# Kernel tuning notes

Measured on AMD Instinct MI355X. Metric: run time of the kernel, lower is better.

The kernel has to match this reference:

```python
import jax, jax.numpy as jnp
import numpy as np

N, E, D = 20000, 640000, 128  # nodes, edges, hidden_nf
ED = 3  # edge_feat_nf (1 input col + distance col + geodesic col)
NORM_FACTOR = 100.0
NORM_CONST = 1.0
LN_EPS = 1e-5


def setup_inputs() -> dict:
    key = jax.random.key(0)
    ks = jax.random.split(key, 24)
    w = lambda k, s: (jax.random.normal(k, s, dtype=jnp.float32) * 0.1)
    inp = {
        "h": jax.random.normal(ks[0], (N, D), dtype=jnp.float32),
        "x": jax.random.normal(ks[1], (N, 3), dtype=jnp.float32),
        "edge_index": jax.random.randint(ks[2], (2, E), 0, N),
        "node_mask": jnp.ones((N, 1), jnp.float32),
        "edge_mask": jnp.ones((E, 1), jnp.float32),
        "edge_attr": jax.random.uniform(ks[3], (E, 1), dtype=jnp.float32),
        # GCLayer params
        "W_lin": w(ks[4], (D, D)), "b_lin": jnp.zeros((D,), jnp.float32),
        "We1": w(ks[5], (D + ED, D)), "be1": jnp.zeros((D,), jnp.float32),
        "We2": w(ks[6], (D, D)), "be2": jnp.zeros((D,), jnp.float32),
        "Wn1": w(ks[7], (D, D)), "bn1": jnp.zeros((D,), jnp.float32),
        "Wn2": w(ks[8], (D, D)), "bn2": jnp.zeros((D,), jnp.float32),
        "Wa1": w(ks[9], (2 * D + ED, D)), "ba1": jnp.zeros((D,), jnp.float32),
        "Wa2": w(ks[10], (D, 1)), "ba2": jnp.zeros((1,), jnp.float32),
        "ln_g": jnp.ones((D,), jnp.float32), "ln_b": jnp.zeros((D,), jnp.float32),
        # EquivariantUpdate coord_mlp params (last layer bias-free, gain 0.001)
        "Wc1": w(ks[11], (2 * D + ED, D)), "bc1": jnp.zeros((D,), jnp.float32),
        "Wc2": w(ks[12], (D, D)), "bc2": jnp.zeros((D,), jnp.float32),
        "Wc3": w(ks[13], (D, 1)) * 0.01,
    }
    return inp


def _forward(h, x, edge_index, node_mask, edge_mask, edge_attr,
             W_lin, b_lin, We1, be1, We2, be2, Wn1, bn1, Wn2, bn2,
             Wa1, ba1, Wa2, ba2, ln_g, ln_b, Wc1, bc1, Wc2, bc2, Wc3):
    silu = jax.nn.silu
    row, col = edge_index[0], edge_index[1]
    # coord2diff
    diff = x[row] - x[col]                                     # [E,3]
    radial = jnp.sum(diff * diff, axis=1, keepdims=True)
    dist = jnp.sqrt(radial + 1e-8)                             # [E,1]
    coord_diff = diff / (dist + NORM_CONST)
    e = jnp.concatenate([dist, edge_attr], axis=1)             # [E,2]
    # ---- GCLayer (Euclidean reduction of HGCLayer) ----
    hh = h @ W_lin + b_lin                                     # [N,D]
    hr, hc = hh[row], hh[col]
    geo = jnp.sqrt(jnp.sum((hr - hc) ** 2, axis=1, keepdims=True) + 1e-8)
    e3 = jnp.concatenate([e, geo], axis=1)                     # [E,3]
    att_in = jnp.concatenate([hr, hc, e3], axis=1)             # [E,2D+3]
    att = jax.nn.sigmoid(silu(att_in @ Wa1 + ba1) @ Wa2 + ba2) * edge_mask
    msg_in = jnp.concatenate([hc - hr, e3], axis=1)            # [E,D+3]
    msg = (silu(msg_in @ We1 + be1) @ We2 + be2) * att
    agg = jax.ops.segment_sum(msg, row, num_segments=hh.shape[0])  # [N,D]
    out = silu(agg @ Wn1 + bn1) @ Wn2 + bn2
    hh = hh + out
    mu = jnp.mean(hh, axis=-1, keepdims=True)
    var = jnp.mean((hh - mu) ** 2, axis=-1, keepdims=True)
    hh = (hh - mu) * jax.lax.rsqrt(var + LN_EPS) * ln_g + ln_b
    hh = silu(hh)
    # ---- EquivariantUpdate (tanh=False) ----
    cin = jnp.concatenate([hh[row], hh[col], e3], axis=1)      # [E,2D+3]
    m = silu(cin @ Wc1 + bc1)
    m = silu(m @ Wc2 + bc2)
    m = m @ Wc3                                                # [E,1]
    trans = coord_diff * m * edge_mask
    aggx = jax.ops.segment_sum(trans, row, num_segments=x.shape[0]) / NORM_FACTOR
    x_out = (x + aggx) * node_mask
    return hh, x_out


def reference(h, x, edge_index, node_mask, edge_mask, edge_attr,
              W_lin, b_lin, We1, be1, We2, be2, Wn1, bn1, Wn2, bn2,
              Wa1, ba1, Wa2, ba2, ln_g, ln_b, Wc1, bc1, Wc2, bc2, Wc3):
    return _forward(h, x, edge_index, node_mask, edge_mask, edge_attr,
                    W_lin, b_lin, We1, be1, We2, be2, Wn1, bn1, Wn2, bn2,
                    Wa1, ba1, Wa2, ba2, ln_g, ln_b, Wc1, bc1, Wc2, bc2, Wc3)
```

## Files before the change

kernel.cpp:

```cpp
#include <hip/hip_runtime.h>
#include <hip/hip_bf16.h>


#define D 128
#define RS 136

typedef unsigned short ushort;
typedef __fp16 half8 __attribute__((ext_vector_type(8)));
typedef __fp16 h16x2 __attribute__((ext_vector_type(2)));
typedef _Float16 f16x2 __attribute__((ext_vector_type(2)));
typedef __attribute__((ext_vector_type(4))) float f32x4;

__device__ __forceinline__ float rcpf(float x) { return __builtin_amdgcn_rcpf(x); }
__device__ __forceinline__ float siluf(float x) { return x * rcpf(1.0f + __expf(-x)); }
__device__ __forceinline__ float sigmf(float x) { return rcpf(1.0f + __expf(-x)); }
__device__ __forceinline__ ushort f2hs(float f) {
    _Float16 h = (_Float16)f; ushort u; __builtin_memcpy(&u, &h, 2); return u;
}
__device__ __forceinline__ unsigned pkh(float lo, float hi) {
    auto h = __builtin_amdgcn_cvt_pkrtz(lo, hi);
    unsigned u; __builtin_memcpy(&u, &h, 4); return u;
}
__device__ __forceinline__ unsigned pksub(unsigned a, unsigned b) {
    f16x2 x, y; __builtin_memcpy(&x, &a, 4); __builtin_memcpy(&y, &b, 4);
    f16x2 d = x - y; unsigned r; __builtin_memcpy(&r, &d, 4); return r;
}
__device__ __forceinline__ float2 up2(unsigned u) {
    f16x2 h; __builtin_memcpy(&h, &u, 4);
    return make_float2((float)h.x, (float)h.y);
}
__device__ __forceinline__ float fdot2f(f16x2 a, f16x2 b, float c) {
#if __has_builtin(__builtin_amdgcn_fdot2)
    h16x2 ah, bh;
    __builtin_memcpy(&ah, &a, 4); __builtin_memcpy(&bh, &b, 4);
    return __builtin_amdgcn_fdot2(ah, bh, c, false);
#else
    return c + (float)a.x * (float)b.x + (float)a.y * (float)b.y;
#endif
}
#define MFMA16(a, b, c) __builtin_amdgcn_mfma_f32_16x16x32_f16((a), (b), (c), 0, 0, 0)

#define PWLIN 0
#define PU    5
#define PV    9
#define PM    13
#define PE2   17
#define PN1   21
#define PN2   26
#define PP    30
#define PQ    34
#define PC2   38
#define NPACK 42

__global__ void k_zero(float* __restrict__ p, long n) {
    long i = (long)blockIdx.x * blockDim.x + threadIdx.x;
    long stride = (long)gridDim.x * blockDim.x;
    for (; i < n; i += stride) p[i] = 0.0f;
}

__global__ void k_hist(const int* __restrict__ eidx, int* __restrict__ cnt, int E) {
    int i = blockIdx.x * blockDim.x + threadIdx.x;
    const int stride = gridDim.x * blockDim.x;
    for (; i < E; i += stride) atomicAdd(&cnt[eidx[i]], 1);
}

__global__ __launch_bounds__(1024) void k_scan(const int* __restrict__ cnt,
                                               int* __restrict__ cur, int N) {
    __shared__ int part[1024];
    const int t = threadIdx.x;
    const int chunk = (N + 1023) / 1024;
    int s = 0;
    for (int k = 0; k < chunk; ++k) {
        const int i = t * chunk + k;
        if (i < N) s += cnt[i];
    }
    part[t] = s;
    __syncthreads();
    for (int d = 1; d < 1024; d <<= 1) {
        const int v = (t >= d) ? part[t - d] : 0;
        __syncthreads();
        part[t] += v;
        __syncthreads();
    }
    int base = (t == 0) ? 0 : part[t - 1];
    for (int k = 0; k < chunk; ++k) {
        const int i = t * chunk + k;
        if (i < N) { cur[i] = base; base += cnt[i]; }
    }
}

__global__ void k_scatter_build(
    const int* __restrict__ eidx, const float* __restrict__ x,
    const float* __restrict__ eattr, const float* __restrict__ emask,
    int* __restrict__ cur, float4* __restrict__ rec, int E) {
    int i = blockIdx.x * blockDim.x + threadIdx.x;
    const int stride = gridDim.x * blockDim.x;
    for (; i < E; i += stride) {
        const int r = eidx[i], c = eidx[E + i];
        const int p = atomicAdd(&cur[r], 1);
        const float dx = x[r * 3 + 0] - x[c * 3 + 0];
        const float dy = x[r * 3 + 1] - x[c * 3 + 1];
        const float dz = x[r * 3 + 2] - x[c * 3 + 2];
        const float dist = sqrtf(dx * dx + dy * dy + dz * dz + 1e-8f);
        const float inv = rcpf(dist + 1.0f);
        rec[2 * p + 0] = make_float4(__int_as_float(r), __int_as_float(c), dist, eattr[i]);
        rec[2 * p + 1] = make_float4(emask[i], dx * inv, dy * inv, dz * inv);
    }
}

__global__ __launch_bounds__(256) void k_packall(
    const float* __restrict__ W_lin, const float* __restrict__ b_lin,
    const float* __restrict__ Wa1,
    const float* __restrict__ We1,
    const float* __restrict__ We2,
    const float* __restrict__ Wn1, const float* __restrict__ bn1,
    const float* __restrict__ Wn2,
    const float* __restrict__ Wc1,
    const float* __restrict__ Wc2,
    ushort* __restrict__ pack) {
    const int b = blockIdx.x, t = threadIdx.x;
    const float* W = nullptr; const float* bias = nullptr;
    int kbase = 0, fold = 0, ext = 0, nW = 0;
    if (b < 5)       { W = W_lin; bias = b_lin; if (b == 4) { ext = 1; nW = 0; } else kbase = b * 32; }
    else if (b < 9)  { W = Wa1; kbase = (b - 5) * 32; fold = 1; }
    else if (b < 13) { W = Wa1; kbase = 128 + (b - 9) * 32; }
    else if (b < 17) { W = We1; kbase = (b - 13) * 32; }
    else if (b < 21) { W = We2; kbase = (b - 17) * 32; }
    else if (b < 26) { int k = b - 21; W = Wn1; bias = bn1; if (k == 4) { ext = 1; nW = 0; } else kbase = k * 32; }
    else if (b < 30) { W = Wn2; kbase = (b - 26) * 32; }
    else if (b < 34) { W = Wc1; kbase = (b - 30) * 32; }
    else if (b < 38) { W = Wc1; kbase = 128 + (b - 34) * 32; }
    else             { W = Wc2; kbase = (b - 38) * 32; }
    ushort* dst = pack + (size_t)b * 4096;
#pragma unroll
    for (int i = 0; i < 16; ++i) {
        const int e = t + 256 * i;
        const int j = e & 7, lane = (e >> 3) & 63, nt = e >> 9;
        const int kl = (lane >> 4) * 8 + j;
        const int n = nt * 16 + (lane & 15);
        float v;
        if (!ext) {
            v = W[(kbase + kl) * D + n];
            if (fold) v += W[(kbase + kl + 128) * D + n];
        } else {
            v = (kl < nW) ? W[(kbase + kl) * D + n] : (kl == nW ? bias[n] : 0.0f);
        }
        dst[e] = f2hs(v);
    }
}

__global__ __launch_bounds__(256) void k_node_lin(
    const float* __restrict__ h, const ushort* __restrict__ pack,
    float* __restrict__ hh, ushort* __restrict__ hh1b,
    float* __restrict__ Uf, ushort* __restrict__ Vh, ushort* __restrict__ Mh,
    const float* __restrict__ ba1f, int N) {
    __shared__ ushort hs[64][RS];
    const int t = threadIdx.x, lane = t & 63, wave = t >> 6;
    const int quad = lane >> 4, l16 = lane & 15;
    const int mh = wave >> 1, nh = wave & 1;
    const int base = blockIdx.x * 64;

#pragma unroll
    for (int q = 0; q < 8; ++q) {
        const int f = t + 256 * q;
        const int row = f >> 5, c4 = (f & 31) << 2;
        const int node = base + row;
        float4 v = make_float4(0.f, 0.f, 0.f, 0.f);
        if (node < N) v = *(const float4*)(h + (size_t)node * D + c4);
        *(uint2*)&hs[row][c4] = make_uint2(pkh(v.x, v.y), pkh(v.z, v.w));
    }
    float ba1v[4];
#pragma unroll
    for (int nt = 0; nt < 4; ++nt) ba1v[nt] = ba1f[nh * 64 + nt * 16 + l16];
    __syncthreads();

    half8 aext = (half8)0;
    if (quad == 0) aext[0] = (__fp16)1.0f;

    f32x4 acc[2][4] = {};
    {
        const half8* pB = (const half8*)(pack + (size_t)PWLIN * 4096);
#pragma unroll
        for (int ks = 0; ks < 5; ++ks) {
            half8 bfr[4];
#pragma unroll
            for (int nt = 0; nt < 4; ++nt) bfr[nt] = pB[(ks * 8 + nh * 4 + nt) * 64 + lane];
#pragma unroll
            for (int mt = 0; mt < 2; ++mt) {
                const half8 a = (ks < 4) ? *(const half8*)&hs[mh * 32 + mt * 16 + l16][ks * 32 + quad * 8]
                                         : aext;
#pragma unroll
                for (int nt = 0; nt < 4; ++nt) acc[mt][nt] = MFMA16(a, bfr[nt], acc[mt][nt]);
            }
        }
    }
    __syncthreads();
#pragma unroll
    for (int mt = 0; mt < 2; ++mt)
#pragma unroll
        for (int reg = 0; reg < 4; ++reg) {
            const int row = mh * 32 + mt * 16 + quad * 4 + reg;
            const int g = base + row;
#pragma unroll
            for (int nt = 0; nt < 4; ++nt) {
                const int col = nh * 64 + nt * 16 + l16;
                const float v = acc[mt][nt][reg];
                const ushort hv = f2hs(v);
                hs[row][col] = hv;
                if (g < N) {
                    hh[(size_t)g * D + col] = v;
                    hh1b[(size_t)g * D + col] = hv;
                }
            }
        }
    __syncthreads();

    {
        f32x4 a2[2][4] = {};
        const half8* pB = (const half8*)(pack + (size_t)PU * 4096);
#pragma unroll
        for (int ks = 0; ks < 4; ++ks) {
            half8 bfr[4];
#pragma unroll
            for (int nt = 0; nt < 4; ++nt) bfr[nt] = pB[(ks * 8 + nh * 4 + nt) * 64 + lane];
#pragma unroll
            for (int mt = 0; mt < 2; ++mt) {
                const half8 a = *(const half8*)&hs[mh * 32 + mt * 16 + l16][ks * 32 + quad * 8];
#pragma unroll
                for (int nt = 0; nt < 4; ++nt) a2[mt][nt] = MFMA16(a, bfr[nt], a2[mt][nt]);
            }
        }
#pragma unroll
        for (int mt = 0; mt < 2; ++mt)
#pragma unroll
            for (int reg = 0; reg < 4; ++reg) {
                const int g = base + mh * 32 + mt * 16 + quad * 4 + reg;
                if (g < N)
#pragma unroll
                    for (int nt = 0; nt < 4; ++nt)
                        Uf[(size_t)g * D + nh * 64 + nt * 16 + l16] = a2[mt][nt][reg] + ba1v[nt];
            }
    }
    {
        f32x4 a2[2][4] = {};
        const half8* pB = (const half8*)(pack + (size_t)PV * 4096);
#pragma unroll
        for (int ks = 0; ks < 4; ++ks) {
            half8 bfr[4];
#pragma unroll
            for (int nt = 0; nt < 4; ++nt) bfr[nt] = pB[(ks * 8 + nh * 4 + nt) * 64 + lane];
#pragma unroll
            for (int mt = 0; mt < 2; ++mt) {
                const half8 a = *(const half8*)&hs[mh * 32 + mt * 16 + l16][ks * 32 + quad * 8];
#pragma unroll
                for (int nt = 0; nt < 4; ++nt) a2[mt][nt] = MFMA16(a, bfr[nt], a2[mt][nt]);
            }
        }
#pragma unroll
        for (int mt = 0; mt < 2; ++mt)
#pragma unroll
            for (int reg = 0; reg < 4; ++reg) {
                const int g = base + mh * 32 + mt * 16 + quad * 4 + reg;
                if (g < N)
#pragma unroll
                    for (int nt = 0; nt < 4; ++nt)
                        Vh[(size_t)g * D + nh * 64 + nt * 16 + l16] = f2hs(a2[mt][nt][reg]);
            }
    }
    {
        f32x4 a2[2][4] = {};
        const half8* pB = (const half8*)(pack + (size_t)PM * 4096);
#pragma unroll
        for (int ks = 0; ks < 4; ++ks) {
            half8 bfr[4];
#pragma unroll
            for (int nt = 0; nt < 4; ++nt) bfr[nt] = pB[(ks * 8 + nh * 4 + nt) * 64 + lane];
#pragma unroll
            for (int mt = 0; mt < 2; ++mt) {
                const half8 a = *(const half8*)&hs[mh * 32 + mt * 16 + l16][ks * 32 + quad * 8];
#pragma unroll
                for (int nt = 0; nt < 4; ++nt) a2[mt][nt] = MFMA16(a, bfr[nt], a2[mt][nt]);
            }
        }
#pragma unroll
        for (int mt = 0; mt < 2; ++mt)
#pragma unroll
            for (int reg = 0; reg < 4; ++reg) {
                const int g = base + mh * 32 + mt * 16 + quad * 4 + reg;
                if (g < N)
#pragma unroll
                    for (int nt = 0; nt < 4; ++nt)
                        Mh[(size_t)g * D + nh * 64 + nt * 16 + l16] = f2hs(a2[mt][nt][reg]);
            }
    }
}

__global__ __launch_bounds__(256, 6) void k_edge1(
    const float4* __restrict__ rec,
    const ushort* __restrict__ hh1b,
    const float*  __restrict__ Uf,
    const ushort* __restrict__ Vh,
    const ushort* __restrict__ Mh,
    const ushort* __restrict__ pack,
    const float* __restrict__ Wa1, const float* __restrict__ We1,
    const float* __restrict__ be1f,
    const float* __restrict__ Wa2f, const float* __restrict__ ba2f,
    const float* __restrict__ be2f,
    float* __restrict__ agg, float* __restrict__ geo_c, int E) {
    __shared__ ushort m1_s[64][RS];
    __shared__ float ew_s[7][128];
    __shared__ float dist_s[64], attr_s[64], geo_s[64], att_s[64], em_s[64];
    __shared__ int node_s[64], col_s[64];

    float (*msg_s)[RS] = (float(*)[RS])&m1_s[0][0];

    const int t = threadIdx.x, lane = t & 63, w = t >> 6;
    const int quad = lane >> 4, l16 = lane & 15;
    const int base = blockIdx.x * 64;

    if (t < 64) {
        const int i = base + t;
        int r = 0, c = 0; float dist = 0.f, at = 0.f, emv = 0.f;
        if (i < E) {
            const float4 ra = rec[2 * i + 0];
            const float4 rb = rec[2 * i + 1];
            r = __float_as_int(ra.x); c = __float_as_int(ra.y);
            dist = ra.z; at = ra.w; emv = rb.x;
        }
        node_s[t] = r; col_s[t] = c;
        dist_s[t] = dist; attr_s[t] = at; em_s[t] = emv;
    }
    for (int i = t; i < 896; i += 256) {
        const int r = i >> 7, c = i & 127;
        float v;
        if (r < 3)      v = Wa1[(256 + r) * D + c];
        else if (r < 6) v = We1[(128 + (r - 3)) * D + c];
        else            v = be1f[c];
        ew_s[r][c] = v;
    }
    float b3[2];
#pragma unroll
    for (int nt = 0; nt < 2; ++nt) b3[nt] = be2f[w * 32 + nt * 16 + l16];
    __syncthreads();

    {
        const int g = t >> 4;
#pragma unroll
        for (int it = 0; it < 4; ++it) {
            const int e = g * 4 + it;
            const uint4 vr = *(const uint4*)(hh1b + (size_t)node_s[e] * D + l16 * 8);
            const uint4 vc = *(const uint4*)(hh1b + (size_t)col_s[e] * D + l16 * 8);
            const unsigned* pr = (const unsigned*)&vr;
            const unsigned* pc = (const unsigned*)&vc;
            float s = 0.f;
#pragma unroll
            for (int q = 0; q < 4; ++q) {
                f16x2 hr2, hc2;
                __builtin_memcpy(&hr2, &pr[q], 4);
                __builtin_memcpy(&hc2, &pc[q], 4);
                const f16x2 d2 = hc2 - hr2;
                s = fdot2f(d2, d2, s);
            }
            s += __shfl_xor(s, 1); s += __shfl_xor(s, 2); s += __shfl_xor(s, 4); s += __shfl_xor(s, 8);
            if (l16 == 0) {
                const float gg = sqrtf(s + 1e-8f);
                geo_s[e] = gg;
                if (base + e < E) geo_c[base + e] = gg;
            }
        }
    }
    __syncthreads();

    {
        const int row = t >> 2, cq = t & 3;
        const int nr = node_s[row], nc = col_s[row];
        const float dist = dist_s[row], attr = attr_s[row], geo = geo_s[row];
        const float*  pU  = Uf + (size_t)nr * D + cq * 32;
        const ushort* pVr = Vh + (size_t)nr * D + cq * 32;
        const ushort* pVc = Vh + (size_t)nc * D + cq * 32;
        const ushort* pMr = Mh + (size_t)nr * D + cq * 32;
        const ushort* pMc = Mh + (size_t)nc * D + cq * 32;
        float p = 0.f;
#pragma unroll
        for (int k4 = 0; k4 < 8; ++k4) {
            const int c4 = cq * 32 + k4 * 4;
            const float4 u  = *(const float4*)(pU + k4 * 4);
            const uint2 vru = *(const uint2*)(pVr + k4 * 4);
            const uint2 vcu = *(const uint2*)(pVc + k4 * 4);
            const uint2 mru = *(const uint2*)(pMr + k4 * 4);
            const uint2 mcu = *(const uint2*)(pMc + k4 * 4);
            const float2 vd01 = up2(pksub(vcu.x, vru.x));
            const float2 vd23 = up2(pksub(vcu.y, vru.y));
            const float2 md01 = up2(pksub(mcu.x, mru.x));
            const float2 md23 = up2(pksub(mcu.y, mru.y));
            const float4 e0 = *(const float4*)&ew_s[0][c4];
            const float4 e1 = *(const float4*)&ew_s[1][c4];
            const float4 e2 = *(const float4*)&ew_s[2][c4];
            const float4 f0 = *(const float4*)&ew_s[3][c4];
            const float4 f1 = *(const float4*)&ew_s[4][c4];
            const float4 f2 = *(const float4*)&ew_s[5][c4];
            const float4 bb = *(const float4*)&ew_s[6][c4];
            const float4 w2 = *(const float4*)(Wa2f + c4);
            const float a0 = u.x + vd01.x + dist * e0.x + attr * e1.x + geo * e2.x;
            const float a1 = u.y + vd01.y + dist * e0.y + attr * e1.y + geo * e2.y;
            const float a2 = u.z + vd23.x + dist * e0.z + attr * e1.z + geo * e2.z;
            const float a3 = u.w + vd23.y + dist * e0.w + attr * e1.w + geo * e2.w;
            p += siluf(a0) * w2.x + siluf(a1) * w2.y + siluf(a2) * w2.z + siluf(a3) * w2.w;
            const float m0 = siluf(md01.x + dist * f0.x + attr * f1.x + geo * f2.x + bb.x);
            const float m1v = siluf(md01.y + dist * f0.y + attr * f1.y + geo * f2.y + bb.y);
            const float m2 = siluf(md23.x + dist * f0.z + attr * f1.z + geo * f2.z + bb.z);
            const float m3 = siluf(md23.y + dist * f0.w + attr * f1.w + geo * f2.w + bb.w);
            *(uint2*)&m1_s[row][c4] = make_uint2(pkh(m0, m1v), pkh(m2, m3));
        }
        p += __shfl_xor(p, 1); p += __shfl_xor(p, 2);
        if (cq == 0) att_s[row] = sigmf(p + ba2f[0]) * em_s[row];
    }
    __syncthreads();

    f32x4 acc3[4][2] = {};
    {
        const half8* pB = (const half8*)(pack + (size_t)PE2 * 4096);
#pragma unroll
        for (int ks = 0; ks < 4; ++ks) {
            const half8 b0 = pB[(ks * 8 + w * 2 + 0) * 64 + lane];
            const half8 b1 = pB[(ks * 8 + w * 2 + 1) * 64 + lane];
#pragma unroll
            for (int mt = 0; mt < 4; ++mt) {
                const half8 a = *(const half8*)&m1_s[mt * 16 + l16][ks * 32 + quad * 8];
                acc3[mt][0] = MFMA16(a, b0, acc3[mt][0]);
                acc3[mt][1] = MFMA16(a, b1, acc3[mt][1]);
            }
        }
    }
    __syncthreads();

#pragma unroll
    for (int pass = 0; pass < 2; ++pass) {
#pragma unroll
        for (int mt = 0; mt < 2; ++mt)
#pragma unroll
            for (int reg = 0; reg < 4; ++reg) {
                const int row = (pass * 2 + mt) * 16 + quad * 4 + reg;
                const float av = att_s[row];
#pragma unroll
                for (int nt = 0; nt < 2; ++nt)
                    msg_s[row - pass * 32][w * 32 + nt * 16 + l16] =
                        (acc3[pass * 2 + mt][nt][reg] + b3[nt]) * av;
            }
        __syncthreads();
        {
            const int j = t & 127, s = t >> 7;
            const int r0 = pass * 32 + s * 16;
            float acc = 0.f;
            int rprev = node_s[r0];
#pragma unroll
            for (int k = 0; k < 16; ++k) {
                const int rn = node_s[r0 + k];
                if (rn != rprev) {
                    atomicAdd(&agg[(size_t)rprev * D + j], acc);
                    acc = 0.f; rprev = rn;
                }
                acc += msg_s[s * 16 + k][j];
            }
            atomicAdd(&agg[(size_t)rprev * D + j], acc);
        }
        __syncthreads();
    }
}

__global__ __launch_bounds__(256) void k_node2(
    const float* __restrict__ agg, float* hio,
    const ushort* __restrict__ pack,
    const float* __restrict__ bn2f,
    const float* __restrict__ ln_g, const float* __restrict__ ln_b,
    const float* __restrict__ bc1f,
    ushort* __restrict__ Ph, ushort* __restrict__ Qh, int N) {
    __shared__ ushort ag_s[64][RS];
    __shared__ float redS[2][64], redQ[2][64];
    const int t = threadIdx.x, lane = t & 63, wave = t >> 6;
    const int quad = lane >> 4, l16 = lane & 15;
    const int mh = wave >> 1, nh = wave & 1;
    const int base = blockIdx.x * 64;

#pragma unroll
    for (int q = 0; q < 8; ++q) {
        const int f = t + 256 * q;
        const int row = f >> 5, c4 = (f & 31) << 2;
        const int node = base + row;
        float4 v = make_float4(0.f, 0.f, 0.f, 0.f);
        if (node < N) v = *(const float4*)(agg + (size_t)node * D + c4);
        *(uint2*)&ag_s[row][c4] = make_uint2(pkh(v.x, v.y), pkh(v.z, v.w));
    }
    float bn2[4], lg[4], lb[4], bc1v[4];
#pragma unroll
    for (int nt = 0; nt < 4; ++nt) {
        const int col = nh * 64 + nt * 16 + l16;
        bn2[nt] = bn2f[col]; lg[nt] = ln_g[col]; lb[nt] = ln_b[col]; bc1v[nt] = bc1f[col];
    }
    __syncthreads();

    half8 aext = (half8)0;
    if (quad == 0) aext[0] = (__fp16)1.0f;

    f32x4 acc[2][4] = {};
    {
        const half8* pB = (const half8*)(pack + (size_t)PN1 * 4096);
#pragma unroll
        for (int ks = 0; ks < 5; ++ks) {
            half8 bfr[4];
#pragma unroll
            for (int nt = 0; nt < 4; ++nt) bfr[nt] = pB[(ks * 8 + nh * 4 + nt) * 64 + lane];
#pragma unroll
            for (int mt = 0; mt < 2; ++mt) {
                const half8 a = (ks < 4) ? *(const half8*)&ag_s[mh * 32 + mt * 16 + l16][ks * 32 + quad * 8]
                                         : aext;
#pragma unroll
                for (int nt = 0; nt < 4; ++nt) acc[mt][nt] = MFMA16(a, bfr[nt], acc[mt][nt]);
            }
        }
    }
    __syncthreads();
#pragma unroll
    for (int mt = 0; mt < 2; ++mt)
#pragma unroll
        for (int reg = 0; reg < 4; ++reg) {
            const int row = mh * 32 + mt * 16 + quad * 4 + reg;
#pragma unroll
            for (int nt = 0; nt < 4; ++nt)
                ag_s[row][nh * 64 + nt * 16 + l16] = f2hs(siluf(acc[mt][nt][reg]));
        }
    __syncthreads();

    {
        const half8* pB = (const half8*)(pack + (size_t)PN2 * 4096);
#pragma unroll
        for (int mt = 0; mt < 2; ++mt)
#pragma unroll
            for (int nt = 0; nt < 4; ++nt) acc[mt][nt] = (f32x4)0.0f;
#pragma unroll
        for (int ks = 0; ks < 4; ++ks) {
            half8 bfr[4];
#pragma unroll
            for (int nt = 0; nt < 4; ++nt) bfr[nt] = pB[(ks * 8 + nh * 4 + nt) * 64 + lane];
#pragma unroll
            for (int mt = 0; mt < 2; ++mt) {
                const half8 a = *(const half8*)&ag_s[mh * 32 + mt * 16 + l16][ks * 32 + quad * 8];
#pragma unroll
                for (int nt = 0; nt < 4; ++nt) acc[mt][nt] = MFMA16(a, bfr[nt], acc[mt][nt]);
            }
        }
    }
#pragma unroll
    for (int mt = 0; mt < 2; ++mt)
#pragma unroll
        for (int reg = 0; reg < 4; ++reg) {
            const int row = mh * 32 + mt * 16 + quad * 4 + reg;
            const int g = base + row;
            float s = 0.f, qq = 0.f;
#pragma unroll
            for (int nt = 0; nt < 4; ++nt) {
                const int col = nh * 64 + nt * 16 + l16;
                float v = acc[mt][nt][reg] + bn2[nt];
                if (g < N) v += hio[(size_t)g * D + col];
                acc[mt][nt][reg] = v;
                s += v; qq += v * v;
            }
            s += __shfl_xor(s, 1); s += __shfl_xor(s, 2); s += __shfl_xor(s, 4); s += __shfl_xor(s, 8);
            qq += __shfl_xor(qq, 1); qq += __shfl_xor(qq, 2); qq += __shfl_xor(qq, 4); qq += __shfl_xor(qq, 8);
            if (l16 == 0) { redS[nh][row] = s; redQ[nh][row] = qq; }
        }
    __syncthreads();

#pragma unroll
    for (int mt = 0; mt < 2; ++mt)
#pragma unroll
        for (int reg = 0; reg < 4; ++reg) {
            const int row = mh * 32 + mt * 16 + quad * 4 + reg;
            const int g = base + row;
            const float mu = (redS[0][row] + redS[1][row]) * (1.0f / D);
            const float var = (redQ[0][row] + redQ[1][row]) * (1.0f / D) - mu * mu;
            const float rstd = rsqrtf(var + 1e-5f);
#pragma unroll
            for (int nt = 0; nt < 4; ++nt) {
                const int col = nh * 64 + nt * 16 + l16;
                const float hn = (acc[mt][nt][reg] - mu) * rstd * lg[nt] + lb[nt];
                const float o = siluf(hn);
                ag_s[row][col] = f2hs(o);
                if (g < N) hio[(size_t)g * D + col] = o;
            }
        }
    __syncthreads();

    {
        f32x4 a2[2][4] = {};
        const half8* pB = (const half8*)(pack + (size_t)PP * 4096);
#pragma unroll
        for (int ks = 0; ks < 4; ++ks) {
            half8 bfr[4];
#pragma unroll
            for (int nt = 0; nt < 4; ++nt) bfr[nt] = pB[(ks * 8 + nh * 4 + nt) * 64 + lane];
#pragma unroll
            for (int mt = 0; mt < 2; ++mt) {
                const half8 a = *(const half8*)&ag_s[mh * 32 + mt * 16 + l16][ks * 32 + quad * 8];
#pragma unroll
                for (int nt = 0; nt < 4; ++nt) a2[mt][nt] = MFMA16(a, bfr[nt], a2[mt][nt]);
            }
        }
#pragma unroll
        for (int mt = 0; mt < 2; ++mt)
#pragma unroll
            for (int reg = 0; reg < 4; ++reg) {
                const int g = base + mh * 32 + mt * 16 + quad * 4 + reg;
                if (g < N)
#pragma unroll
                    for (int nt = 0; nt < 4; ++nt)
                        Ph[(size_t)g * D + nh * 64 + nt * 16 + l16] = f2hs(a2[mt][nt][reg] + bc1v[nt]);
            }
    }
    {
        f32x4 a2[2][4] = {};
        const half8* pB = (const half8*)(pack + (size_t)PQ * 4096);
#pragma unroll
        for (int ks = 0; ks < 4; ++ks) {
            half8 bfr[4];
#pragma unroll
            for (int nt = 0; nt < 4; ++nt) bfr[nt] = pB[(ks * 8 + nh * 4 + nt) * 64 + lane];
#pragma unroll
            for (int mt = 0; mt < 2; ++mt) {
                const half8 a = *(const half8*)&ag_s[mh * 32 + mt * 16 + l16][ks * 32 + quad * 8];
#pragma unroll
                for (int nt = 0; nt < 4; ++nt) a2[mt][nt] = MFMA16(a, bfr[nt], a2[mt][nt]);
            }
        }
#pragma unroll
        for (int mt = 0; mt < 2; ++mt)
#pragma unroll
            for (int reg = 0; reg < 4; ++reg) {
                const int g = base + mh * 32 + mt * 16 + quad * 4 + reg;
                if (g < N)
#pragma unroll
                    for (int nt = 0; nt < 4; ++nt)
                        Qh[(size_t)g * D + nh * 64 + nt * 16 + l16] = f2hs(a2[mt][nt][reg]);
            }
    }
}

__global__ __launch_bounds__(256, 6) void k_edge2(
    const float4* __restrict__ rec, const float* __restrict__ geo_c,
    const ushort* __restrict__ Ph, const ushort* __restrict__ Qh,
    const ushort* __restrict__ pack,
    const float* __restrict__ Wc1,
    const float* __restrict__ bc2f, const float* __restrict__ Wc3f,
    float* __restrict__ aggx, int E) {
    __shared__ ushort c1_s[64][RS];
    __shared__ float ew_s[3][128];
    __shared__ float dist_s[64], attr_s[64], geo_s[64], tr_s[64];
    __shared__ float cdx_s[64], cdy_s[64], cdz_s[64];
    __shared__ int node_s[64], col_s[64];
    __shared__ float mp_s[4][64];

    const int t = threadIdx.x, lane = t & 63, w = t >> 6;
    const int quad = lane >> 4, l16 = lane & 15;
    const int base = blockIdx.x * 64;

    if (t < 64) {
        const int i = base + t;
        int r = 0, c = 0;
        float dist = 1.f, geo = 0.f, at = 0.f, emv = 0.f, cdx = 0.f, cdy = 0.f, cdz = 0.f;
        if (i < E) {
            const float4 ra = rec[2 * i + 0];
            const float4 rb = rec[2 * i + 1];
            r = __float_as_int(ra.x); c = __float_as_int(ra.y);
            dist = ra.z; at = ra.w;
            emv = rb.x; cdx = rb.y; cdy = rb.z; cdz = rb.w;
            geo = geo_c[i];
        }
        node_s[t] = r; col_s[t] = c;
        dist_s[t] = dist; geo_s[t] = geo; attr_s[t] = at; tr_s[t] = emv;
        cdx_s[t] = cdx; cdy_s[t] = cdy; cdz_s[t] = cdz;
    }
    for (int i = t; i < 384; i += 256) {
        const int r = i >> 7, c = i & 127;
        ew_s[r][c] = Wc1[(256 + r) * D + c];
    }
    float bc2[2], wc3[2];
#pragma unroll
    for (int nt = 0; nt < 2; ++nt) {
        const int col = w * 32 + nt * 16 + l16;
        bc2[nt] = bc2f[col]; wc3[nt] = Wc3f[col];
    }
    __syncthreads();

    {
        const int row = t >> 2, cq = t & 3;
        const int nr = node_s[row], nc = col_s[row];
        const float dist = dist_s[row], attr = attr_s[row], geo = geo_s[row];
        const ushort* pP = Ph + (size_t)nr * D + cq * 32;
        const ushort* pQ = Qh + (size_t)nc * D + cq * 32;
#pragma unroll
        for (int k4 = 0; k4 < 8; ++k4) {
            const int c4 = cq * 32 + k4 * 4;
            const uint2 pu = *(const uint2*)(pP + k4 * 4);
            const uint2 qu = *(const uint2*)(pQ + k4 * 4);
            const float2 p01 = up2(pu.x), p23 = up2(pu.y);
            const float2 q01 = up2(qu.x), q23 = up2(qu.y);
            const float4 e0 = *(const float4*)&ew_s[0][c4];
            const float4 e1 = *(const float4*)&ew_s[1][c4];
            const float4 e2 = *(const float4*)&ew_s[2][c4];
            const float c0 = siluf(p01.x + q01.x + dist * e0.x + attr * e1.x + geo * e2.x);
            const float c1 = siluf(p01.y + q01.y + dist * e0.y + attr * e1.y + geo * e2.y);
            const float c2 = siluf(p23.x + q23.x + dist * e0.z + attr * e1.z + geo * e2.z);
            const float c3 = siluf(p23.y + q23.y + dist * e0.w + attr * e1.w + geo * e2.w);
            *(uint2*)&c1_s[row][c4] = make_uint2(pkh(c0, c1), pkh(c2, c3));
        }
    }
    __syncthreads();

    {
        f32x4 acc[4][2] = {};
        const half8* pB = (const half8*)(pack + (size_t)PC2 * 4096);
#pragma unroll
        for (int ks = 0; ks < 4; ++ks) {
            const half8 b0 = pB[(ks * 8 + w * 2 + 0) * 64 + lane];
            const half8 b1 = pB[(ks * 8 + w * 2 + 1) * 64 + lane];
#pragma unroll
            for (int mt = 0; mt < 4; ++mt) {
                const half8 a = *(const half8*)&c1_s[mt * 16 + l16][ks * 32 + quad * 8];
                acc[mt][0] = MFMA16(a, b0, acc[mt][0]);
                acc[mt][1] = MFMA16(a, b1, acc[mt][1]);
            }
        }
#pragma unroll
        for (int mt = 0; mt < 4; ++mt)
#pragma unroll
            for (int reg = 0; reg < 4; ++reg) {
                float p = siluf(acc[mt][0][reg] + bc2[0]) * wc3[0]
                        + siluf(acc[mt][1][reg] + bc2[1]) * wc3[1];
                p += __shfl_xor(p, 1); p += __shfl_xor(p, 2); p += __shfl_xor(p, 4); p += __shfl_xor(p, 8);
                if (l16 == 0) mp_s[w][mt * 16 + quad * 4 + reg] = p;
            }
    }
    __syncthreads();

    if (t < 64) {
        const float m = mp_s[0][t] + mp_s[1][t] + mp_s[2][t] + mp_s[3][t];
        tr_s[t] = m * tr_s[t];
        if (base + t >= E) tr_s[t] = 0.f;
    }
    __syncthreads();

    {
        const int h = t >> 7, tt = t & 127;
        if (tt < 3) {
            const float* cds = (tt == 0) ? cdx_s : (tt == 1) ? cdy_s : cdz_s;
            float acc = 0.f;
            int rprev = node_s[h * 32];
#pragma unroll
            for (int k = 0; k < 32; ++k) {
                const int row = h * 32 + k;
                const int rn = node_s[row];
                if (rn != rprev) {
                    atomicAdd(&aggx[rprev * 4 + tt], acc);
                    acc = 0.f; rprev = rn;
                }
                acc += cds[row] * tr_s[row];
            }
            atomicAdd(&aggx[rprev * 4 + tt], acc);
        }
    }
}

__global__ void k_coord(const float* __restrict__ x, const float* __restrict__ nmask,
                        const float* __restrict__ aggx, float* __restrict__ out_x, int N) {
    const int idx = blockIdx.x * blockDim.x + threadIdx.x;
    if (idx >= N * 3) return;
    const int i = idx / 3, d = idx - i * 3;
    out_x[idx] = (x[idx] + aggx[i * 4 + d] * (1.0f / 100.0f)) * nmask[i];
}

extern "C" void kernel_launch(void* const* d_in, const int* in_sizes, int n_in,
                              void* d_out, int out_size, void* d_ws, size_t ws_size,
                              hipStream_t stream) {
    const float* h     = (const float*)d_in[0];
    const float* x     = (const float*)d_in[1];
    const int*   eidx  = (const int*)d_in[2];
    const float* nmask = (const float*)d_in[3];
    const float* emask = (const float*)d_in[4];
    const float* eattr = (const float*)d_in[5];
    const float* W_lin = (const float*)d_in[6];
    const float* b_lin = (const float*)d_in[7];
    const float* We1   = (const float*)d_in[8];
    const float* be1   = (const float*)d_in[9];
    const float* We2   = (const float*)d_in[10];
    const float* be2   = (const float*)d_in[11];
    const float* Wn1   = (const float*)d_in[12];
    const float* bn1   = (const float*)d_in[13];
    const float* Wn2   = (const float*)d_in[14];
    const float* bn2   = (const float*)d_in[15];
    const float* Wa1   = (const float*)d_in[16];
    const float* ba1   = (const float*)d_in[17];
    const float* Wa2   = (const float*)d_in[18];
    const float* ba2   = (const float*)d_in[19];
    const float* ln_g  = (const float*)d_in[20];
    const float* ln_b  = (const float*)d_in[21];
    const float* Wc1   = (const float*)d_in[22];
    const float* bc1   = (const float*)d_in[23];
    const float* Wc2   = (const float*)d_in[24];
    const float* bc2   = (const float*)d_in[25];
    const float* Wc3   = (const float*)d_in[26];

    const int N = in_sizes[0] / D;
    const int E = in_sizes[2] / 2;

    char* wp = (char*)d_ws;
    auto take = [&](size_t bytes) -> void* {
        void* p = wp; wp += (bytes + 255) & ~(size_t)255; return p;
    };
    float*  agg   = (float*)take((size_t)N * D * 4);
    float*  aggx  = (float*)take((size_t)N * 4 * 4);
    int*    cnt   = (int*)take((size_t)N * 4);
    int*    cur   = (int*)take((size_t)N * 4);
    float4* rec   = (float4*)take((size_t)E * 32);
    float*  geo_c = (float*)take((size_t)E * 4);
    ushort* hh1b  = (ushort*)take((size_t)N * D * 2);
    float*  Uf    = (float*)take((size_t)N * D * 4);
    ushort* Vh    = (ushort*)take((size_t)N * D * 2);
    ushort* Mh    = (ushort*)take((size_t)N * D * 2);
    ushort* Ph    = (ushort*)take((size_t)N * D * 2);
    ushort* Qh    = (ushort*)take((size_t)N * D * 2);
    ushort* pack  = (ushort*)take((size_t)NPACK * 4096 * 2);

    float* out_h = (float*)d_out;
    float* out_x = out_h + (size_t)N * D;

    const int EB = (E + 63) / 64;
    const int NB = (N + 63) / 64;
    const long zn = ((char*)(cnt + N) - (char*)agg) / 4;

    k_zero<<<2048, 256, 0, stream>>>(agg, zn);
    k_packall<<<NPACK, 256, 0, stream>>>(W_lin, b_lin, Wa1, We1, We2,
                                         Wn1, bn1, Wn2, Wc1, Wc2, pack);
    k_hist<<<1024, 256, 0, stream>>>(eidx, cnt, E);
    k_scan<<<1, 1024, 0, stream>>>(cnt, cur, N);
    k_scatter_build<<<1024, 256, 0, stream>>>(eidx, x, eattr, emask, cur, rec, E);
    k_node_lin<<<NB, 256, 0, stream>>>(h, pack, out_h, hh1b, Uf, Vh, Mh, ba1, N);
    k_edge1<<<EB, 256, 0, stream>>>(rec, hh1b, Uf, Vh, Mh, pack, Wa1, We1, be1,
                                    Wa2, ba2, be2, agg, geo_c, E);
    k_node2<<<NB, 256, 0, stream>>>(agg, out_h, pack, bn2, ln_g, ln_b, bc1, Ph, Qh, N);
    k_edge2<<<EB, 256, 0, stream>>>(rec, geo_c, Ph, Qh, pack, Wc1, bc2, Wc3, aggx, E);
    k_coord<<<(N * 3 + 255) / 256, 256, 0, stream>>>(x, nmask, aggx, out_x, N);
}
```

Before: 493.0 us.

## Store per-node edge projections as fp16 with signs and bias folded in

The fp32 row projection U is replaced by an fp16 buffer Vp, and a negated, bias-folded copy Mp is added. Each edge then does a single packed fp16 add of row and column terms instead of a subtraction plus a separate fp32 load and bias add. The per-block LDS staging of the small edge-feature weight rows is removed in favour of direct global (cached) loads, and the occupancy hints for both edge kernels are raised. This cuts gather bytes per edge and LDS use, in exchange for more fp16 rounding error and an extra node-side buffer write.

```diff
diff --git a/kernel.cpp b/kernel.cpp
--- a/kernel.cpp
+++ b/kernel.cpp
@@ -21,9 +21,9 @@
     auto h = __builtin_amdgcn_cvt_pkrtz(lo, hi);
     unsigned u; __builtin_memcpy(&u, &h, 4); return u;
 }
-__device__ __forceinline__ unsigned pksub(unsigned a, unsigned b) {
+__device__ __forceinline__ unsigned pkadd(unsigned a, unsigned b) {
     f16x2 x, y; __builtin_memcpy(&x, &a, 4); __builtin_memcpy(&y, &b, 4);
-    f16x2 d = x - y; unsigned r; __builtin_memcpy(&r, &d, 4); return r;
+    f16x2 d = x + y; unsigned r; __builtin_memcpy(&r, &d, 4); return r;
 }
 __device__ __forceinline__ float2 up2(unsigned u) {
     f16x2 h; __builtin_memcpy(&h, &u, 4);
@@ -122,7 +122,7 @@
     const float* W = nullptr; const float* bias = nullptr;
     int kbase = 0, fold = 0, ext = 0, nW = 0;
     if (b < 5)       { W = W_lin; bias = b_lin; if (b == 4) { ext = 1; nW = 0; } else kbase = b * 32; }
-    else if (b < 9)  { W = Wa1; kbase = (b - 5) * 32; fold = 1; }
+    else if (b < 9)  { W = Wa1; kbase = (b - 5) * 32; }
     else if (b < 13) { W = Wa1; kbase = 128 + (b - 9) * 32; }
     else if (b < 17) { W = We1; kbase = (b - 13) * 32; }
     else if (b < 21) { W = We2; kbase = (b - 17) * 32; }
@@ -152,8 +152,9 @@
 __global__ __launch_bounds__(256) void k_node_lin(
     const float* __restrict__ h, const ushort* __restrict__ pack,
     float* __restrict__ hh, ushort* __restrict__ hh1b,
-    float* __restrict__ Uf, ushort* __restrict__ Vh, ushort* __restrict__ Mh,
-    const float* __restrict__ ba1f, int N) {
+    ushort* __restrict__ Vp, ushort* __restrict__ Vh,
+    ushort* __restrict__ Mp, ushort* __restrict__ Mh,
+    const float* __restrict__ ba1f, const float* __restrict__ be1f, int N) {
     __shared__ ushort hs[64][RS];
     const int t = threadIdx.x, lane = t & 63, wave = t >> 6;
     const int quad = lane >> 4, l16 = lane & 15;
@@ -169,9 +170,12 @@
         if (node < N) v = *(const float4*)(h + (size_t)node * D + c4);
         *(uint2*)&hs[row][c4] = make_uint2(pkh(v.x, v.y), pkh(v.z, v.w));
     }
-    float ba1v[4];
-#pragma unroll
-    for (int nt = 0; nt < 4; ++nt) ba1v[nt] = ba1f[nh * 64 + nt * 16 + l16];
+    float ba1v[4], be1v[4];
+#pragma unroll
+    for (int nt = 0; nt < 4; ++nt) {
+        const int col = nh * 64 + nt * 16 + l16;
+        ba1v[nt] = ba1f[col]; be1v[nt] = be1f[col];
+    }
     __syncthreads();
 
     half8 aext = (half8)0;
@@ -238,7 +242,7 @@
                 if (g < N)
 #pragma unroll
                     for (int nt = 0; nt < 4; ++nt)
-                        Uf[(size_t)g * D + nh * 64 + nt * 16 + l16] = a2[mt][nt][reg] + ba1v[nt];
+                        Vp[(size_t)g * D + nh * 64 + nt * 16 + l16] = f2hs(a2[mt][nt][reg] + ba1v[nt]);
             }
     }
     {
@@ -289,26 +293,27 @@
                 const int g = base + mh * 32 + mt * 16 + quad * 4 + reg;
                 if (g < N)
 #pragma unroll
-                    for (int nt = 0; nt < 4; ++nt)
-                        Mh[(size_t)g * D + nh * 64 + nt * 16 + l16] = f2hs(a2[mt][nt][reg]);
-            }
-    }
-}
-
-__global__ __launch_bounds__(256, 6) void k_edge1(
+                    for (int nt = 0; nt < 4; ++nt) {
+                        const int col = nh * 64 + nt * 16 + l16;
+                        const float v = a2[mt][nt][reg];
+                        Mh[(size_t)g * D + col] = f2hs(v);
+                        Mp[(size_t)g * D + col] = f2hs(be1v[nt] - v);
+                    }
+            }
+    }
+}
+
+__global__ __launch_bounds__(256, 8) void k_edge1(
     const float4* __restrict__ rec,
     const ushort* __restrict__ hh1b,
-    const float*  __restrict__ Uf,
-    const ushort* __restrict__ Vh,
-    const ushort* __restrict__ Mh,
+    const ushort* __restrict__ Vp, const ushort* __restrict__ Vh,
+    const ushort* __restrict__ Mp, const ushort* __restrict__ Mh,
     const ushort* __restrict__ pack,
     const float* __restrict__ Wa1, const float* __restrict__ We1,
-    const float* __restrict__ be1f,
     const float* __restrict__ Wa2f, const float* __restrict__ ba2f,
     const float* __restrict__ be2f,
     float* __restrict__ agg, float* __restrict__ geo_c, int E) {
     __shared__ ushort m1_s[64][RS];
-    __shared__ float ew_s[7][128];
     __shared__ float dist_s[64], attr_s[64], geo_s[64], att_s[64], em_s[64];
     __shared__ int node_s[64], col_s[64];
 
@@ -330,14 +335,6 @@
         node_s[t] = r; col_s[t] = c;
         dist_s[t] = dist; attr_s[t] = at; em_s[t] = emv;
     }
-    for (int i = t; i < 896; i += 256) {
-        const int r = i >> 7, c = i & 127;
-        float v;
-        if (r < 3)      v = Wa1[(256 + r) * D + c];
-        else if (r < 6) v = We1[(128 + (r - 3)) * D + c];
-        else            v = be1f[c];
-        ew_s[r][c] = v;
-    }
     float b3[2];
 #pragma unroll
     for (int nt = 0; nt < 2; ++nt) b3[nt] = be2f[w * 32 + nt * 16 + l16];
@@ -375,41 +372,40 @@
         const int row = t >> 2, cq = t & 3;
         const int nr = node_s[row], nc = col_s[row];
         const float dist = dist_s[row], attr = attr_s[row], geo = geo_s[row];
-        const float*  pU  = Uf + (size_t)nr * D + cq * 32;
-        const ushort* pVr = Vh + (size_t)nr * D + cq * 32;
+        const ushort* pVr = Vp + (size_t)nr * D + cq * 32;
         const ushort* pVc = Vh + (size_t)nc * D + cq * 32;
-        const ushort* pMr = Mh + (size_t)nr * D + cq * 32;
+        const ushort* pMr = Mp + (size_t)nr * D + cq * 32;
         const ushort* pMc = Mh + (size_t)nc * D + cq * 32;
+        const float* Wa1x = Wa1 + 256 * D;
+        const float* We1x = We1 + 128 * D;
         float p = 0.f;
 #pragma unroll
         for (int k4 = 0; k4 < 8; ++k4) {
             const int c4 = cq * 32 + k4 * 4;
-            const float4 u  = *(const float4*)(pU + k4 * 4);
             const uint2 vru = *(const uint2*)(pVr + k4 * 4);
             const uint2 vcu = *(const uint2*)(pVc + k4 * 4);
             const uint2 mru = *(const uint2*)(pMr + k4 * 4);
             const uint2 mcu = *(const uint2*)(pMc + k4 * 4);
-            const float2 vd01 = up2(pksub(vcu.x, vru.x));
-            const float2 vd23 = up2(pksub(vcu.y, vru.y));
-            const float2 md01 = up2(pksub(mcu.x, mru.x));
-            const float2 md23 = up2(pksub(mcu.y, mru.y));
-            const float4 e0 = *(const float4*)&ew_s[0][c4];
-            const float4 e1 = *(const float4*)&ew_s[1][c4];
-            const float4 e2 = *(const float4*)&ew_s[2][c4];
-            const float4 f0 = *(const float4*)&ew_s[3][c4];
-            const float4 f1 = *(const float4*)&ew_s[4][c4];
-            const float4 f2 = *(const float4*)&ew_s[5][c4];
-            const float4 bb = *(const float4*)&ew_s[6][c4];
+            const float2 av01 = up2(pkadd(vru.x, vcu.x));
+            const float2 av23 = up2(pkadd(vru.y, vcu.y));
+            const float2 mv01 = up2(pkadd(mru.x, mcu.x));
+            const float2 mv23 = up2(pkadd(mru.y, mcu.y));
+            const float4 e0 = *(const float4*)(Wa1x + c4);
+            const float4 e1 = *(const float4*)(Wa1x + D + c4);
+            const float4 e2 = *(const float4*)(Wa1x + 2 * D + c4);
+            const float4 f0 = *(const float4*)(We1x + c4);
+            const float4 f1 = *(const float4*)(We1x + D + c4);
+            const float4 f2 = *(const float4*)(We1x + 2 * D + c4);
             const float4 w2 = *(const float4*)(Wa2f + c4);
-            const float a0 = u.x + vd01.x + dist * e0.x + attr * e1.x + geo * e2.x;
-            const float a1 = u.y + vd01.y + dist * e0.y + attr * e1.y + geo * e2.y;
-            const float a2 = u.z + vd23.x + dist * e0.z + attr * e1.z + geo * e2.z;
-            const float a3 = u.w + vd23.y + dist * e0.w + attr * e1.w + geo * e2.w;
+            const float a0 = av01.x + dist * e0.x + attr * e1.x + geo * e2.x;
+            const float a1 = av01.y + dist * e0.y + attr * e1.y + geo * e2.y;
+            const float a2 = av23.x + dist * e0.z + attr * e1.z + geo * e2.z;
+            const float a3 = av23.y + dist * e0.w + attr * e1.w + geo * e2.w;
             p += siluf(a0) * w2.x + siluf(a1) * w2.y + siluf(a2) * w2.z + siluf(a3) * w2.w;
-            const float m0 = siluf(md01.x + dist * f0.x + attr * f1.x + geo * f2.x + bb.x);
-            const float m1v = siluf(md01.y + dist * f0.y + attr * f1.y + geo * f2.y + bb.y);
-            const float m2 = siluf(md23.x + dist * f0.z + attr * f1.z + geo * f2.z + bb.z);
-            const float m3 = siluf(md23.y + dist * f0.w + attr * f1.w + geo * f2.w + bb.w);
+            const float m0 = siluf(mv01.x + dist * f0.x + attr * f1.x + geo * f2.x);
+            const float m1v = siluf(mv01.y + dist * f0.y + attr * f1.y + geo * f2.y);
+            const float m2 = siluf(mv23.x + dist * f0.z + attr * f1.z + geo * f2.z);
+            const float m3 = siluf(mv23.y + dist * f0.w + attr * f1.w + geo * f2.w);
             *(uint2*)&m1_s[row][c4] = make_uint2(pkh(m0, m1v), pkh(m2, m3));
         }
         p += __shfl_xor(p, 1); p += __shfl_xor(p, 2);
@@ -645,7 +641,7 @@
     }
 }
 
-__global__ __launch_bounds__(256, 6) void k_edge2(
+__global__ __launch_bounds__(256, 7) void k_edge2(
     const float4* __restrict__ rec, const float* __restrict__ geo_c,
     const ushort* __restrict__ Ph, const ushort* __restrict__ Qh,
     const ushort* __restrict__ pack,
@@ -653,7 +649,6 @@
     const float* __restrict__ bc2f, const float* __restrict__ Wc3f,
     float* __restrict__ aggx, int E) {
     __shared__ ushort c1_s[64][RS];
-    __shared__ float ew_s[3][128];
     __shared__ float dist_s[64], attr_s[64], geo_s[64], tr_s[64];
     __shared__ float cdx_s[64], cdy_s[64], cdz_s[64];
     __shared__ int node_s[64], col_s[64];
@@ -679,10 +674,6 @@
         dist_s[t] = dist; geo_s[t] = geo; attr_s[t] = at; tr_s[t] = emv;
         cdx_s[t] = cdx; cdy_s[t] = cdy; cdz_s[t] = cdz;
     }
-    for (int i = t; i < 384; i += 256) {
-        const int r = i >> 7, c = i & 127;
-        ew_s[r][c] = Wc1[(256 + r) * D + c];
-    }
     float bc2[2], wc3[2];
 #pragma unroll
     for (int nt = 0; nt < 2; ++nt) {
@@ -697,20 +688,21 @@
         const float dist = dist_s[row], attr = attr_s[row], geo = geo_s[row];
         const ushort* pP = Ph + (size_t)nr * D + cq * 32;
         const ushort* pQ = Qh + (size_t)nc * D + cq * 32;
+        const float* Wc1x = Wc1 + 256 * D;
 #pragma unroll
         for (int k4 = 0; k4 < 8; ++k4) {
             const int c4 = cq * 32 + k4 * 4;
             const uint2 pu = *(const uint2*)(pP + k4 * 4);
             const uint2 qu = *(const uint2*)(pQ + k4 * 4);
-            const float2 p01 = up2(pu.x), p23 = up2(pu.y);
-            const float2 q01 = up2(qu.x), q23 = up2(qu.y);
-            const float4 e0 = *(const float4*)&ew_s[0][c4];
-            const float4 e1 = *(const float4*)&ew_s[1][c4];
-            const float4 e2 = *(const float4*)&ew_s[2][c4];
-            const float c0 = siluf(p01.x + q01.x + dist * e0.x + attr * e1.x + geo * e2.x);
-            const float c1 = siluf(p01.y + q01.y + dist * e0.y + attr * e1.y + geo * e2.y);
-            const float c2 = siluf(p23.x + q23.x + dist * e0.z + attr * e1.z + geo * e2.z);
-            const float c3 = siluf(p23.y + q23.y + dist * e0.w + attr * e1.w + geo * e2.w);
+            const float2 s01 = up2(pkadd(pu.x, qu.x));
+            const float2 s23 = up2(pkadd(pu.y, qu.y));
+            const float4 e0 = *(const float4*)(Wc1x + c4);
+            const float4 e1 = *(const float4*)(Wc1x + D + c4);
+            const float4 e2 = *(const float4*)(Wc1x + 2 * D + c4);
+            const float c0 = siluf(s01.x + dist * e0.x + attr * e1.x + geo * e2.x);
+            const float c1 = siluf(s01.y + dist * e0.y + attr * e1.y + geo * e2.y);
+            const float c2 = siluf(s23.x + dist * e0.z + attr * e1.z + geo * e2.z);
+            const float c3 = siluf(s23.y + dist * e0.w + attr * e1.w + geo * e2.w);
             *(uint2*)&c1_s[row][c4] = make_uint2(pkh(c0, c1), pkh(c2, c3));
         }
     }
@@ -823,8 +815,9 @@
     float4* rec   = (float4*)take((size_t)E * 32);
     float*  geo_c = (float*)take((size_t)E * 4);
     ushort* hh1b  = (ushort*)take((size_t)N * D * 2);
-    float*  Uf    = (float*)take((size_t)N * D * 4);
+    ushort* Vp    = (ushort*)take((size_t)N * D * 2);
     ushort* Vh    = (ushort*)take((size_t)N * D * 2);
+    ushort* Mp    = (ushort*)take((size_t)N * D * 2);
     ushort* Mh    = (ushort*)take((size_t)N * D * 2);
     ushort* Ph    = (ushort*)take((size_t)N * D * 2);
     ushort* Qh    = (ushort*)take((size_t)N * D * 2);
@@ -843,8 +836,8 @@
     k_hist<<<1024, 256, 0, stream>>>(eidx, cnt, E);
     k_scan<<<1, 1024, 0, stream>>>(cnt, cur, N);
     k_scatter_build<<<1024, 256, 0, stream>>>(eidx, x, eattr, emask, cur, rec, E);
-    k_node_lin<<<NB, 256, 0, stream>>>(h, pack, out_h, hh1b, Uf, Vh, Mh, ba1, N);
-    k_edge1<<<EB, 256, 0, stream>>>(rec, hh1b, Uf, Vh, Mh, pack, Wa1, We1, be1,
+    k_node_lin<<<NB, 256, 0, stream>>>(h, pack, out_h, hh1b, Vp, Vh, Mp, Mh, ba1, be1, N);
+    k_edge1<<<EB, 256, 0, stream>>>(rec, hh1b, Vp, Vh, Mp, Mh, pack, Wa1, We1,
                                     Wa2, ba2, be2, agg, geo_c, E);
     k_node2<<<NB, 256, 0, stream>>>(agg, out_h, pack, bn2, ln_g, ln_b, bc1, Ph, Qh, N);
     k_edge2<<<EB, 256, 0, stream>>>(rec, geo_c, Ph, Qh, pack, Wc1, bc2, Wc3, aggx, E);
```

Result: slower. 742.5 us (+50.6%).
